# Kernel optimization log

Measured on AMD Instinct MI355X. Metric: run time of the kernel, lower is better.

The kernel has to match this reference:

```python
import jax, jax.numpy as jnp
import numpy as np

EPS = 1e-5  # pyg LayerNorm default eps


def _graph_ln(x):
    # pyg.nn.norm.LayerNorm(affine=False), default mode='graph', batch=None:
    # normalizes over ALL elements of the tensor (x - x.mean()) / x.std(unbiased=False)
    m = x.mean()
    v = jnp.mean((x - m) ** 2)
    return (x - m) * jax.lax.rsqrt(v + EPS)


def _cheb_conv(x, row, col, w, W, b):
    # ChebConv, normalization='sym', lambda_max=2 => scaled Laplacian
    # L_hat = L - I = -D^{-1/2} A D^{-1/2} (self-loops removed, weighted)
    # x: [B,N,C_in], row/col: [E], w: [E], W: [K,C_in,C_out], b: [C_out]
    N = x.shape[1]
    w = jnp.where(row == col, 0.0, w)  # remove_self_loops
    deg = jnp.zeros((N,), x.dtype).at[row].add(w)
    dinv = jnp.where(deg > 0, jax.lax.rsqrt(jnp.maximum(deg, 1e-12)), 0.0)
    norm = -(dinv[row] * w * dinv[col])  # [E]

    def prop(t):  # out[i] += norm_e * t[j] for edge (j=row -> i=col)
        msg = norm[None, :, None] * t[:, row, :]  # [B,E,C]
        return jnp.zeros_like(t).at[:, col, :].add(msg)

    Tx0 = x
    out = jnp.einsum('bnc,cd->bnd', Tx0, W[0])
    Tx1 = prop(x)
    out = out + jnp.einsum('bnc,cd->bnd', Tx1, W[1])
    for k in range(2, W.shape[0]):
        Tx2 = 2.0 * prop(Tx1) - Tx0
        out = out + jnp.einsum('bnc,cd->bnd', Tx2, W[k])
        Tx0, Tx1 = Tx1, Tx2
    return out + b


def setup_inputs() -> dict:
    key = jax.random.key(0)
    ks = jax.random.split(key, 8)
    B, N, C, E, L, K = 8, 2048, 256, 32768, 3, 3
    node_feature = jax.random.normal(ks[0], (B, N, C), dtype=jnp.float32)
    edge_index = jax.random.randint(ks[1], (L, 2, E), 0, N)
    edge_weight = jax.random.uniform(ks[2], (L, E), dtype=jnp.float32)
    s = 1.0 / np.sqrt(C)
    cheb_w = jax.random.normal(ks[3], (L, K, C, C), dtype=jnp.float32) * s
    cheb_b = jnp.zeros((L, C), dtype=jnp.float32)
    mlp_w = jax.random.normal(ks[4], (L, C, C), dtype=jnp.float32) * s
    mlp_b = jax.random.normal(ks[5], (L, C), dtype=jnp.float32) * 0.01
    return {"node_feature": node_feature, "edge_weight": edge_weight,
            "cheb_w": cheb_w, "cheb_b": cheb_b, "mlp_w": mlp_w,
            "mlp_b": mlp_b, "edge_index": edge_index}


def reference(node_feature, edge_weight, cheb_w, cheb_b, mlp_w, mlp_b, edge_index):
    h = node_feature  # [B,N,C]
    L = cheb_w.shape[0]
    for l in range(L):
        h_res = h
        hn = _graph_ln(h)
        hc = _cheb_conv(hn, edge_index[l, 0], edge_index[l, 1],
                        edge_weight[l], cheb_w[l], cheb_b[l])
        h = hc + h_res
        h_res = h
        hn = _graph_ln(h)
        hm = jax.nn.gelu(jnp.einsum('bnc,cd->bnd', hn, mlp_w[l]) + mlp_b[l],
                         approximate=False)  # dropout is identity at inference
        h = hm + h_res
    return h.mean(axis=1)  # [B,C]
```

## Files before the change

### kernel.cpp

```cpp
#include <hip/hip_runtime.h>

#define BATCH   8
#define NNODE   2048
#define CH      256
#define NEDGE   32768
#define NLAYER  3
#define MROWS   (NNODE*BATCH)
#define KCAT    (3*CH)
#define NTOT    (MROWS*CH)

typedef _Float16 half8 __attribute__((ext_vector_type(8)));
typedef _Float16 half4 __attribute__((ext_vector_type(4)));
typedef float    f32x4 __attribute__((ext_vector_type(4)));

#define OFF_H      ((size_t)0)
#define OFF_ACAT   ((size_t)16777216)
#define OFF_HF     ((size_t)41943040)
#define OFF_WT     ((size_t)50331648)
#define OFF_MT     ((size_t)51511296)
#define OFF_PARTA  ((size_t)51904512)
#define OFF_PARTB  ((size_t)51912704)
#define OFF_CS     ((size_t)51920896)
#define OFF_CSM    ((size_t)51930112)
#define OFF_DEG    ((size_t)51933184)
#define OFF_CNT    ((size_t)51957760)
#define OFF_ELIST  ((size_t)51982336)
#define OFF_NORM   ((size_t)53555200)
#define OFF_R1     ((size_t)53948416)
#define OFF_R2     ((size_t)53972992)
#define OFF_MP     ((size_t)53997568)

__device__ __forceinline__ void async_lds16(const void* g, void* l) {
  __builtin_amdgcn_global_load_lds((const __attribute__((address_space(1))) void*)g,
                                   (__attribute__((address_space(3))) void*)l, 16, 0, 0);
}

__global__ __launch_bounds__(256) void k_init(const float* __restrict__ x,
                                              float* __restrict__ h,
                                              _Float16* __restrict__ Acat,
                                              float2* __restrict__ part,
                                              float* __restrict__ deg,
                                              unsigned int* __restrict__ count,
                                              float* __restrict__ r1) {
  const int blk = blockIdx.x;
  if (blk < 1024) {
    int tid = blk*256 + threadIdx.x;
    float s = 0.f, s2 = 0.f;
    for (int i = tid; i < NTOT/4; i += 1024*256) {
      int c4 = i & 63, b = (i >> 6) & 7, n = i >> 9;
      float4 v = ((const float4*)x)[((b*NNODE + n) << 6) + c4];
      ((float4*)h)[i] = v;
      half4 o; o[0]=(_Float16)v.x; o[1]=(_Float16)v.y; o[2]=(_Float16)v.z; o[3]=(_Float16)v.w;
      *(half4*)&Acat[(size_t)(i >> 6)*KCAT + c4*4] = o;
      s  += v.x + v.y + v.z + v.w;
      s2 += v.x*v.x + v.y*v.y + v.z*v.z + v.w*v.w;
    }
    __shared__ float rs[512];
    rs[threadIdx.x] = s; rs[256+threadIdx.x] = s2; __syncthreads();
    for (int o = 128; o > 0; o >>= 1) {
      if (threadIdx.x < o) { rs[threadIdx.x] += rs[threadIdx.x+o]; rs[256+threadIdx.x] += rs[256+threadIdx.x+o]; }
      __syncthreads();
    }
    if (threadIdx.x == 0) part[blk] = make_float2(rs[0], rs[256]);
  } else {
    int i = (blk - 1024)*256 + threadIdx.x;
    if (i < NLAYER*NNODE) { deg[i] = 0.f; count[i] = 0u; r1[i] = 0.f; }
  }
}

__global__ __launch_bounds__(256) void k_weights(const float* __restrict__ cheb_w,
                                                 const float* __restrict__ mlp_w,
                                                 _Float16* __restrict__ Wt,
                                                 _Float16* __restrict__ Mt) {
  __shared__ _Float16 lt[64][72];
  const int t = threadIdx.x;
  const int rr = t >> 4, c4 = t & 15;
  const int tile = blockIdx.x;
  if (tile < 144) {
    const int l = tile / 48, rem = tile % 48;
    const int kk = rem / 16, q = rem % 16, ci = q >> 2, ni = q & 3;
    const float4* W  = (const float4*)cheb_w + ((size_t)((l*3 + kk)*CH + ci*64))*64 + ni*16;
    const float4* W2 = (const float4*)cheb_w + ((size_t)((l*3 + 2 )*CH + ci*64))*64 + ni*16;
    #pragma unroll
    for (int p = 0; p < 4; ++p) {
      const int r = p*16 + rr;
      float4 v = W[(size_t)r*64 + c4];
      if (kk == 0) {
        float4 v2 = W2[(size_t)r*64 + c4];
        v.x -= v2.x; v.y -= v2.y; v.z -= v2.z; v.w -= v2.w;
      } else if (kk == 2) {
        v.x *= 2.f; v.y *= 2.f; v.z *= 2.f; v.w *= 2.f;
      }
      lt[c4*4+0][r] = (_Float16)v.x; lt[c4*4+1][r] = (_Float16)v.y;
      lt[c4*4+2][r] = (_Float16)v.z; lt[c4*4+3][r] = (_Float16)v.w;
    }
    __syncthreads();
    const int nr = t >> 2, ch2 = t & 3;
    #pragma unroll
    for (int pp = 0; pp < 2; ++pp) {
      const int ch = ch2 + pp*4;
      half8 v = *(const half8*)&lt[nr][ch*8];
      *(half8*)&Wt[((size_t)(l*CH + ni*64 + nr))*KCAT + kk*256 + ci*64 + ch*8] = v;
    }
  } else {
    const int m = tile - 144;
    const int l = m / 16, q = m % 16, ci = q >> 2, ni = q & 3;
    const float4* W = (const float4*)mlp_w + ((size_t)(l*CH + ci*64))*64 + ni*16;
    #pragma unroll
    for (int p = 0; p < 4; ++p) {
      const int r = p*16 + rr;
      float4 v = W[(size_t)r*64 + c4];
      lt[c4*4+0][r] = (_Float16)v.x; lt[c4*4+1][r] = (_Float16)v.y;
      lt[c4*4+2][r] = (_Float16)v.z; lt[c4*4+3][r] = (_Float16)v.w;
    }
    __syncthreads();
    const int nr = t >> 2, ch2 = t & 3;
    #pragma unroll
    for (int pp = 0; pp < 2; ++pp) {
      const int ch = ch2 + pp*4;
      half8 v = *(const half8*)&lt[nr][ch*8];
      *(half8*)&Mt[((size_t)(l*CH + ni*64 + nr))*CH + ci*64 + ch*8] = v;
    }
  }
}

__global__ __launch_bounds__(256) void k_edge_scatter(const int* __restrict__ ei,
                                                      const float* __restrict__ ew,
                                                      float* deg, unsigned int* count,
                                                      unsigned int* elist) {
  int i = blockIdx.x*256 + threadIdx.x;
  if (i >= NLAYER*NEDGE) return;
  int l = i / NEDGE, e = i % NEDGE;
  const int* rows = ei + l*2*NEDGE;
  const int* cols = rows + NEDGE;
  int r = rows[e], c = cols[e];
  float w = (r == c) ? 0.f : ew[l*NEDGE + e];
  atomicAdd(&deg[l*NNODE + r], w);
  unsigned int slot = atomicAdd(&count[l*NNODE + c], 1u);
  if (slot < 64u) elist[(l*NNODE + c)*64 + slot] = (unsigned int)e;
}

__global__ __launch_bounds__(256) void k_edge_norm(const int* __restrict__ ei,
                                                   const float* __restrict__ ew,
                                                   const float* __restrict__ deg,
                                                   float* __restrict__ norm,
                                                   float* __restrict__ r1) {
  int i = blockIdx.x*256 + threadIdx.x;
  if (i >= NLAYER*NEDGE) return;
  int l = i / NEDGE, e = i % NEDGE;
  const int* rows = ei + l*2*NEDGE;
  const int* cols = rows + NEDGE;
  int r = rows[e], c = cols[e];
  float w = (r == c) ? 0.f : ew[l*NEDGE + e];
  float dr = deg[l*NNODE + r], dc = deg[l*NNODE + c];
  float ir = dr > 0.f ? rsqrtf(fmaxf(dr, 1e-12f)) : 0.f;
  float ic = dc > 0.f ? rsqrtf(fmaxf(dc, 1e-12f)) : 0.f;
  float nm = -(ir * w * ic);
  norm[i] = nm;
  atomicAdd(&r1[l*NNODE + c], nm);
}

__global__ __launch_bounds__(256) void k_aux(const int* __restrict__ ei,
                                             const float* __restrict__ norm,
                                             const unsigned int* __restrict__ count,
                                             const unsigned int* __restrict__ elist,
                                             const float* __restrict__ r1,
                                             float* __restrict__ r2,
                                             const _Float16* __restrict__ Wt,
                                             const _Float16* __restrict__ Mt,
                                             float* __restrict__ cs,
                                             float* __restrict__ csM) {
  const int blk = blockIdx.x;
  if (blk < 24) {
    int i = blk*256 + threadIdx.x;
    int l = i / NNODE;
    const int* rows = ei + l*2*NEDGE;
    unsigned int c = count[i]; if (c > 64u) c = 64u;
    const unsigned int* el = elist + (size_t)i*64;
    float s = 0.f;
    for (unsigned int j = 0; j < c; ++j) {
      unsigned int e = el[j];
      s += norm[l*NEDGE + e] * r1[l*NNODE + rows[e]];
    }
    r2[i] = s;
  } else if (blk < 33) {
    int idx = blk - 24;
    int l = idx / 3, kk = idx % 3, n = threadIdx.x;
    const half8* row = (const half8*)&Wt[((size_t)(l*CH + n))*KCAT + kk*256];
    float s = 0.f;
    #pragma unroll 4
    for (int j = 0; j < 32; ++j) {
      half8 v = row[j];
      s += (float)v[0]+(float)v[1]+(float)v[2]+(float)v[3]
         + (float)v[4]+(float)v[5]+(float)v[6]+(float)v[7];
    }
    cs[(l*3 + kk)*CH + n] = s;
  } else {
    int l = blk - 33, n = threadIdx.x;
    const half8* row = (const half8*)&Mt[((size_t)(l*CH + n))*CH];
    float s = 0.f;
    #pragma unroll 4
    for (int j = 0; j < 32; ++j) {
      half8 v = row[j];
      s += (float)v[0]+(float)v[1]+(float)v[2]+(float)v[3]
         + (float)v[4]+(float)v[5]+(float)v[6]+(float)v[7];
    }
    csM[l*CH + n] = s;
  }
}

template<int SRC_OFF, int DST_OFF>
__global__ __launch_bounds__(64) void k_prop(_Float16* __restrict__ Acat,
                                             const int* __restrict__ rows,
                                             const float* __restrict__ norm,
                                             const unsigned int* __restrict__ count,
                                             const unsigned int* __restrict__ elist) {
  const int blk = blockIdx.x;
  const int b = blk & 7, dst = blk >> 3;
  const int lane = threadIdx.x;
  unsigned int cnt = count[dst]; if (cnt > 64u) cnt = 64u;
  int   srcv = 0;
  float nmv  = 0.f;
  if (lane < (int)cnt) {
    unsigned int e = elist[dst*64 + lane];
    srcv = rows[e];
    nmv  = norm[e];
  }
  float a0 = 0.f, a1 = 0.f, a2 = 0.f, a3 = 0.f;
  const _Float16* base = Acat + SRC_OFF + lane*4;
  #define PROP_STEP(i)                                                              \
    {                                                                               \
      int   src = __builtin_amdgcn_readlane(srcv, (i));                             \
      int   nbi = __builtin_amdgcn_readlane(__builtin_bit_cast(int, nmv), (i));     \
      float nm  = __builtin_bit_cast(float, nbi);                                   \
      half4 v = *(const half4*)&base[(size_t)(src*8 + b)*KCAT];                     \
      a0 += nm*(float)v[0]; a1 += nm*(float)v[1];                                   \
      a2 += nm*(float)v[2]; a3 += nm*(float)v[3];                                   \
    }
  unsigned int i = 0;
  for (; i + 4 <= cnt; i += 4) { PROP_STEP(i) PROP_STEP(i+1) PROP_STEP(i+2) PROP_STEP(i+3) }
  for (; i < cnt; ++i) { PROP_STEP(i) }
  #undef PROP_STEP
  half4 o; o[0] = (_Float16)a0; o[1] = (_Float16)a1; o[2] = (_Float16)a2; o[3] = (_Float16)a3;
  *(half4*)&Acat[(size_t)(dst*8 + b)*KCAT + DST_OFF + lane*4] = o;
}

template<int KSTEPS, int DO_GELU>
__global__ __launch_bounds__(256) void k_gemm(const _Float16* __restrict__ A, int lda,
                                              const _Float16* __restrict__ Bt, int ldb,
                                              const float* __restrict__ bias,
                                              const float* __restrict__ cs,
                                              const float* __restrict__ r1,
                                              const float* __restrict__ r2,
                                              const float2* __restrict__ part_in,
                                              float2* __restrict__ part_out,
                                              float* __restrict__ H,
                                              _Float16* __restrict__ Of, int ofs) {
  __shared__ _Float16 Als[64*64];
  __shared__ _Float16 Bls[64*64];
  __shared__ float red[512];
  __shared__ float mv[2];
  const int bm = blockIdx.x, bn = blockIdx.y;
  const int t = threadIdx.x;
  const int w = t >> 6, lane = t & 63;
  const int quad = lane >> 4, l16 = lane & 15;
  const int wm = w & 1, wn = w >> 1;

  {
    float s = 0.f, s2 = 0.f;
    for (int i = t; i < 1024; i += 256) { float2 p = part_in[i]; s += p.x; s2 += p.y; }
    red[t] = s; red[256+t] = s2; __syncthreads();
    for (int o = 128; o > 0; o >>= 1) {
      if (t < o) { red[t] += red[t+o]; red[256+t] += red[256+t+o]; }
      __syncthreads();
    }
    if (t == 0) {
      float mean = red[0] * (1.f/(float)NTOT);
      float var  = red[256] * (1.f/(float)NTOT) - mean*mean;
      mv[0] = mean; mv[1] = rsqrtf(var + 1e-5f);
    }
    __syncthreads();
  }
  const float mean = mv[0], istd = mv[1];

  f32x4 acc00 = {0.f,0.f,0.f,0.f};
  f32x4 acc01 = acc00, acc10 = acc00, acc11 = acc00;

  const int c0 = w*64 + lane, c1 = 256 + w*64 + lane;
  const int r0 = c0 >> 3, s0 = (c0 & 7) ^ (r0 & 7);
  const int r1i = c1 >> 3, s1 = (c1 & 7) ^ (r1i & 7);
  const _Float16* ga0 = A  + (size_t)(bm*64 + r0)*lda + s0*8;
  const _Float16* ga1 = A  + (size_t)(bm*64 + r1i)*lda + s1*8;
  const _Float16* gb0 = Bt + (size_t)(bn*64 + r0)*ldb + s0*8;
  const _Float16* gb1 = Bt + (size_t)(bn*64 + r1i)*ldb + s1*8;
  _Float16* lA0 = &Als[w*512];
  _Float16* lA1 = &Als[2048 + w*512];
  _Float16* lB0 = &Bls[w*512];
  _Float16* lB1 = &Bls[2048 + w*512];

  const int ra0 = wm*32 + l16, ra1 = ra0 + 16;
  const int rb0 = wn*32 + l16, rb1 = rb0 + 16;

  for (int ks = 0; ks < KSTEPS; ++ks) {
    async_lds16(ga0, lA0); async_lds16(ga1, lA1);
    async_lds16(gb0, lB0); async_lds16(gb1, lB1);
    ga0 += 64; ga1 += 64; gb0 += 64; gb1 += 64;
    __syncthreads();
    #pragma unroll
    for (int kh = 0; kh < 2; ++kh) {
      const int q = kh*4 + quad;
      half8 a0 = *(const half8*)&Als[ra0*64 + (q ^ (ra0 & 7))*8];
      half8 a1 = *(const half8*)&Als[ra1*64 + (q ^ (ra1 & 7))*8];
      half8 b0 = *(const half8*)&Bls[rb0*64 + (q ^ (rb0 & 7))*8];
      half8 b1 = *(const half8*)&Bls[rb1*64 + (q ^ (rb1 & 7))*8];
      acc00 = __builtin_amdgcn_mfma_f32_16x16x32_f16(a0, b0, acc00, 0, 0, 0);
      acc01 = __builtin_amdgcn_mfma_f32_16x16x32_f16(a0, b1, acc01, 0, 0, 0);
      acc10 = __builtin_amdgcn_mfma_f32_16x16x32_f16(a1, b0, acc10, 0, 0, 0);
      acc11 = __builtin_amdgcn_mfma_f32_16x16x32_f16(a1, b1, acc11, 0, 0, 0);
    }
    __syncthreads();
  }

  float s = 0.f, s2 = 0.f;
  const int gm0 = bm*64 + wm*32, gn0 = bn*64 + wn*32;
  const float mi = -mean * istd;
  #pragma unroll
  for (int i = 0; i < 2; ++i) {
    #pragma unroll
    for (int j = 0; j < 2; ++j) {
      f32x4 a = (i == 0) ? (j == 0 ? acc00 : acc01) : (j == 0 ? acc10 : acc11);
      const int col = gn0 + j*16 + l16;
      const float bv = bias[col];
      const float c0v = cs[col];
      float c1v = 0.f, c2v = 0.f;
      if (!DO_GELU) { c1v = cs[256 + col]; c2v = cs[512 + col]; }
      #pragma unroll
      for (int r = 0; r < 4; ++r) {
        const int row = gm0 + i*16 + quad*4 + r;
        float v;
        if (DO_GELU) {
          v = istd*a[r] + mi*c0v + bv;
          v = 0.5f*v*(1.f + erff(v*0.70710678118654752f));
        } else {
          const int node = row >> 3;
          v = istd*a[r] + mi*(c0v + r1[node]*c1v + r2[node]*c2v) + bv;
        }
        float hv = H[(size_t)row*CH + col] + v;
        H[(size_t)row*CH + col] = hv;
        Of[(size_t)row*ofs + col] = (_Float16)hv;
        s += hv; s2 += hv*hv;
      }
    }
  }
  red[t] = s; red[256+t] = s2; __syncthreads();
  for (int o = 128; o > 0; o >>= 1) {
    if (t < o) { red[t] += red[t+o]; red[256+t] += red[256+t+o]; }
    __syncthreads();
  }
  if (t == 0) part_out[blockIdx.y*gridDim.x + blockIdx.x] = make_float2(red[0], red[256]);
}

__global__ __launch_bounds__(256) void k_mean_part(const float* __restrict__ h,
                                                   float* __restrict__ mp) {
  int blk = blockIdx.x;
  int b = blk & 7, chunk = blk >> 3;
  int c = threadIdx.x;
  float s = 0.f;
  for (int k = 0; k < 32; ++k) {
    int n = chunk*32 + k;
    s += h[((size_t)(n*8 + b) << 8) + c];
  }
  mp[((b*64 + chunk) << 8) + c] = s;
}

__global__ __launch_bounds__(256) void k_mean_final(const float* __restrict__ mp,
                                                    float* __restrict__ out) {
  int b = blockIdx.x, c = threadIdx.x;
  float s = 0.f;
  for (int ch = 0; ch < 64; ++ch) s += mp[((b*64 + ch) << 8) + c];
  out[(b << 8) + c] = s * (1.f/(float)NNODE);
}

extern "C" void kernel_launch(void* const* d_in, const int* in_sizes, int n_in,
                              void* d_out, int out_size, void* d_ws, size_t ws_size,
                              hipStream_t stream) {
  const float* x      = (const float*)d_in[0];
  const float* ew     = (const float*)d_in[1];
  const float* cheb_w = (const float*)d_in[2];
  const float* cheb_b = (const float*)d_in[3];
  const float* mlp_w  = (const float*)d_in[4];
  const float* mlp_b  = (const float*)d_in[5];
  const int*   ei     = (const int*)d_in[6];
  float* out = (float*)d_out;

  char* ws = (char*)d_ws;
  float*        h     = (float*)(ws + OFF_H);
  _Float16*     Acat  = (_Float16*)(ws + OFF_ACAT);
  _Float16*     Hf    = (_Float16*)(ws + OFF_HF);
  _Float16*     Wt    = (_Float16*)(ws + OFF_WT);
  _Float16*     Mt    = (_Float16*)(ws + OFF_MT);
  float2*       partA = (float2*)(ws + OFF_PARTA);
  float2*       partB = (float2*)(ws + OFF_PARTB);
  float*        cs    = (float*)(ws + OFF_CS);
  float*        csM   = (float*)(ws + OFF_CSM);
  float*        deg   = (float*)(ws + OFF_DEG);
  unsigned int* cnt   = (unsigned int*)(ws + OFF_CNT);
  unsigned int* elist = (unsigned int*)(ws + OFF_ELIST);
  float*        norm  = (float*)(ws + OFF_NORM);
  float*        r1    = (float*)(ws + OFF_R1);
  float*        r2    = (float*)(ws + OFF_R2);
  float*        mp    = (float*)(ws + OFF_MP);

  k_init<<<1048, 256, 0, stream>>>(x, h, Acat, partA, deg, cnt, r1);
  k_weights<<<192, 256, 0, stream>>>(cheb_w, mlp_w, Wt, Mt);
  k_edge_scatter<<<(NLAYER*NEDGE)/256, 256, 0, stream>>>(ei, ew, deg, cnt, elist);
  k_edge_norm<<<(NLAYER*NEDGE)/256, 256, 0, stream>>>(ei, ew, deg, norm, r1);
  k_aux<<<36, 256, 0, stream>>>(ei, norm, cnt, elist, r1, r2, Wt, Mt, cs, csM);

  for (int l = 0; l < NLAYER; ++l) {
    const int* rows_l = ei + l*2*NEDGE;
    const unsigned int* cnt_l = cnt + l*NNODE;
    const unsigned int* el_l  = elist + (size_t)l*NNODE*64;
    const float* norm_l = norm + l*NEDGE;

    k_prop<0, 256><<<MROWS, 64, 0, stream>>>(Acat, rows_l, norm_l, cnt_l, el_l);
    k_prop<256, 512><<<MROWS, 64, 0, stream>>>(Acat, rows_l, norm_l, cnt_l, el_l);
    k_gemm<12, 0><<<dim3(256, 4), 256, 0, stream>>>(
        Acat, KCAT, Wt + (size_t)l*CH*KCAT, KCAT, cheb_b + l*CH,
        cs + l*3*CH, r1 + l*NNODE, r2 + l*NNODE, partA, partB, h, Hf, CH);
    k_gemm<4, 1><<<dim3(256, 4), 256, 0, stream>>>(
        Hf, CH, Mt + (size_t)l*CH*CH, CH, mlp_b + l*CH,
        csM + l*CH, r1, r2, partB, partA, h, Acat, KCAT);
  }

  k_mean_part<<<512, 256, 0, stream>>>(h, mp);
  k_mean_final<<<8, 256, 0, stream>>>(mp, out);
}
```

Before: 317.3 us.

## Drop fp32 residual buffer, read residual from fp16, batch-group prop, merge weight prep

Removes the fp32 hidden-state buffer h. Residuals are now read from the fp16 copies already held in Acat and Hf, and the mean is taken from Acat, which cuts global read/write traffic in the GEMM epilogues. k_prop now has each wavefront handle four batches of one destination node, with 256-thread blocks, so the edge-list and readlane setup is shared. The weight-transpose kernel is folded into k_init to save a launch. The residual stream is now kept only in fp16, so rounding error builds up across layers.

```diff
diff --git a/kernel.cpp b/kernel.cpp
--- a/kernel.cpp
+++ b/kernel.cpp
@@ -13,22 +13,21 @@
 typedef _Float16 half4 __attribute__((ext_vector_type(4)));
 typedef float    f32x4 __attribute__((ext_vector_type(4)));
 
-#define OFF_H      ((size_t)0)
-#define OFF_ACAT   ((size_t)16777216)
-#define OFF_HF     ((size_t)41943040)
-#define OFF_WT     ((size_t)50331648)
-#define OFF_MT     ((size_t)51511296)
-#define OFF_PARTA  ((size_t)51904512)
-#define OFF_PARTB  ((size_t)51912704)
-#define OFF_CS     ((size_t)51920896)
-#define OFF_CSM    ((size_t)51930112)
-#define OFF_DEG    ((size_t)51933184)
-#define OFF_CNT    ((size_t)51957760)
-#define OFF_ELIST  ((size_t)51982336)
-#define OFF_NORM   ((size_t)53555200)
-#define OFF_R1     ((size_t)53948416)
-#define OFF_R2     ((size_t)53972992)
-#define OFF_MP     ((size_t)53997568)
+#define OFF_ACAT   ((size_t)0)
+#define OFF_HF     ((size_t)25165824)
+#define OFF_WT     ((size_t)33554432)
+#define OFF_MT     ((size_t)34734080)
+#define OFF_PARTA  ((size_t)35127296)
+#define OFF_PARTB  ((size_t)35135488)
+#define OFF_CS     ((size_t)35143680)
+#define OFF_CSM    ((size_t)35152896)
+#define OFF_DEG    ((size_t)35155968)
+#define OFF_CNT    ((size_t)35180544)
+#define OFF_ELIST  ((size_t)35205120)
+#define OFF_NORM   ((size_t)36777984)
+#define OFF_R1     ((size_t)37171200)
+#define OFF_R2     ((size_t)37195776)
+#define OFF_MP     ((size_t)37220352)
 
 __device__ __forceinline__ void async_lds16(const void* g, void* l) {
   __builtin_amdgcn_global_load_lds((const __attribute__((address_space(1))) void*)g,
@@ -36,90 +35,86 @@
 }
 
 __global__ __launch_bounds__(256) void k_init(const float* __restrict__ x,
-                                              float* __restrict__ h,
                                               _Float16* __restrict__ Acat,
                                               float2* __restrict__ part,
+                                              const float* __restrict__ cheb_w,
+                                              const float* __restrict__ mlp_w,
+                                              _Float16* __restrict__ Wt,
+                                              _Float16* __restrict__ Mt,
                                               float* __restrict__ deg,
                                               unsigned int* __restrict__ count,
                                               float* __restrict__ r1) {
-  const int blk = blockIdx.x;
+  __shared__ float rs[512];
+  __shared__ _Float16 lt[64][72];
+  const int blk = blockIdx.x, t = threadIdx.x;
   if (blk < 1024) {
-    int tid = blk*256 + threadIdx.x;
+    int tid = blk*256 + t;
     float s = 0.f, s2 = 0.f;
     for (int i = tid; i < NTOT/4; i += 1024*256) {
       int c4 = i & 63, b = (i >> 6) & 7, n = i >> 9;
       float4 v = ((const float4*)x)[((b*NNODE + n) << 6) + c4];
-      ((float4*)h)[i] = v;
       half4 o; o[0]=(_Float16)v.x; o[1]=(_Float16)v.y; o[2]=(_Float16)v.z; o[3]=(_Float16)v.w;
       *(half4*)&Acat[(size_t)(i >> 6)*KCAT + c4*4] = o;
       s  += v.x + v.y + v.z + v.w;
       s2 += v.x*v.x + v.y*v.y + v.z*v.z + v.w*v.w;
     }
-    __shared__ float rs[512];
-    rs[threadIdx.x] = s; rs[256+threadIdx.x] = s2; __syncthreads();
+    rs[t] = s; rs[256+t] = s2; __syncthreads();
     for (int o = 128; o > 0; o >>= 1) {
-      if (threadIdx.x < o) { rs[threadIdx.x] += rs[threadIdx.x+o]; rs[256+threadIdx.x] += rs[256+threadIdx.x+o]; }
+      if (t < o) { rs[t] += rs[t+o]; rs[256+t] += rs[256+t+o]; }
       __syncthreads();
     }
-    if (threadIdx.x == 0) part[blk] = make_float2(rs[0], rs[256]);
+    if (t == 0) part[blk] = make_float2(rs[0], rs[256]);
+  } else if (blk < 1048) {
+    int i = (blk - 1024)*256 + t;
+    if (i < NLAYER*NNODE) { deg[i] = 0.f; count[i] = 0u; r1[i] = 0.f; }
   } else {
-    int i = (blk - 1024)*256 + threadIdx.x;
-    if (i < NLAYER*NNODE) { deg[i] = 0.f; count[i] = 0u; r1[i] = 0.f; }
-  }
-}
-
-__global__ __launch_bounds__(256) void k_weights(const float* __restrict__ cheb_w,
-                                                 const float* __restrict__ mlp_w,
-                                                 _Float16* __restrict__ Wt,
-                                                 _Float16* __restrict__ Mt) {
-  __shared__ _Float16 lt[64][72];
-  const int t = threadIdx.x;
-  const int rr = t >> 4, c4 = t & 15;
-  const int tile = blockIdx.x;
-  if (tile < 144) {
-    const int l = tile / 48, rem = tile % 48;
-    const int kk = rem / 16, q = rem % 16, ci = q >> 2, ni = q & 3;
-    const float4* W  = (const float4*)cheb_w + ((size_t)((l*3 + kk)*CH + ci*64))*64 + ni*16;
-    const float4* W2 = (const float4*)cheb_w + ((size_t)((l*3 + 2 )*CH + ci*64))*64 + ni*16;
-    #pragma unroll
-    for (int p = 0; p < 4; ++p) {
-      const int r = p*16 + rr;
-      float4 v = W[(size_t)r*64 + c4];
-      if (kk == 0) {
-        float4 v2 = W2[(size_t)r*64 + c4];
-        v.x -= v2.x; v.y -= v2.y; v.z -= v2.z; v.w -= v2.w;
-      } else if (kk == 2) {
-        v.x *= 2.f; v.y *= 2.f; v.z *= 2.f; v.w *= 2.f;
+    const int tile = blk - 1048;
+    const int rr = t >> 4, c4 = t & 15;
+    if (tile < 144) {
+      const int l = tile / 48, rem = tile % 48;
+      const int kk = rem / 16, q = rem % 16, ci = q >> 2, ni = q & 3;
+      const float4* W  = (const float4*)cheb_w + ((size_t)((l*3 + kk)*CH + ci*64))*64 + ni*16;
+      const float4* W2 = (const float4*)cheb_w + ((size_t)((l*3 + 2 )*CH + ci*64))*64 + ni*16;
+      #pragma unroll
+      for (int p = 0; p < 4; ++p) {
+        const int r = p*16 + rr;
+        float4 v = W[(size_t)r*64 + c4];
+        if (kk == 0) {
+          float4 v2 = W2[(size_t)r*64 + c4];
+          v.x -= v2.x; v.y -= v2.y; v.z -= v2.z; v.w -= v2.w;
+        } else if (kk == 2) {
+          v.x *= 2.f; v.y *= 2.f; v.z *= 2.f; v.w *= 2.f;
+        }
+        lt[c4*4+0][r] = (_Float16)v.x; lt[c4*4+1][r] = (_Float16)v.y;
+        lt[c4*4+2][r] = (_Float16)v.z; lt[c4*4+3][r] = (_Float16)v.w;
       }
-      lt[c4*4+0][r] = (_Float16)v.x; lt[c4*4+1][r] = (_Float16)v.y;
-      lt[c4*4+2][r] = (_Float16)v.z; lt[c4*4+3][r] = (_Float16)v.w;
-    }
-    __syncthreads();
-    const int nr = t >> 2, ch2 = t & 3;
-    #pragma unroll
-    for (int pp = 0; pp < 2; ++pp) {
-      const int ch = ch2 + pp*4;
-      half8 v = *(const half8*)&lt[nr][ch*8];
-      *(half8*)&Wt[((size_t)(l*CH + ni*64 + nr))*KCAT + kk*256 + ci*64 + ch*8] = v;
-    }
-  } else {
-    const int m = tile - 144;
-    const int l = m / 16, q = m % 16, ci = q >> 2, ni = q & 3;
-    const float4* W = (const float4*)mlp_w + ((size_t)(l*CH + ci*64))*64 + ni*16;
-    #pragma unroll
-    for (int p = 0; p < 4; ++p) {
-      const int r = p*16 + rr;
-      float4 v = W[(size_t)r*64 + c4];
-      lt[c4*4+0][r] = (_Float16)v.x; lt[c4*4+1][r] = (_Float16)v.y;
-      lt[c4*4+2][r] = (_Float16)v.z; lt[c4*4+3][r] = (_Float16)v.w;
-    }
-    __syncthreads();
-    const int nr = t >> 2, ch2 = t & 3;
-    #pragma unroll
-    for (int pp = 0; pp < 2; ++pp) {
-      const int ch = ch2 + pp*4;
-      half8 v = *(const half8*)&lt[nr][ch*8];
-      *(half8*)&Mt[((size_t)(l*CH + ni*64 + nr))*CH + ci*64 + ch*8] = v;
+      __syncthreads();
+      const int nr = t >> 2, ch2 = t & 3;
+      #pragma unroll
+      for (int pp = 0; pp < 2; ++pp) {
+        const int ch = ch2 + pp*4;
+        half8 v = *(const half8*)&lt[nr][ch*8];
+        *(half8*)&Wt[((size_t)(l*CH + ni*64 + nr))*KCAT + kk*256 + ci*64 + ch*8] = v;
+      }
+    } else {
+      const int m = tile - 144;
+      const int l = m / 16, q = m % 16, ci = q >> 2, ni = q & 3;
+      const float4* W = (const float4*)mlp_w + ((size_t)(l*CH + ci*64))*64 + ni*16;
+      #pragma unroll
+      for (int p = 0; p < 4; ++p) {
+        const int r = p*16 + rr;
+        float4 v = W[(size_t)r*64 + c4];
+        lt[c4*4+0][r] = (_Float16)v.x; lt[c4*4+1][r] = (_Float16)v.y;
+        lt[c4*4+2][r] = (_Float16)v.z; lt[c4*4+3][r] = (_Float16)v.w;
+      }
+      __syncthreads();
+      const int nr = t >> 2, ch2 = t & 3;
+      #pragma unroll
+      for (int pp = 0; pp < 2; ++pp) {
+        const int ch = ch2 + pp*4;
+        half8 v = *(const half8*)&lt[nr][ch*8];
+        *(half8*)&Mt[((size_t)(l*CH + ni*64 + nr))*CH + ci*64 + ch*8] = v;
+      }
     }
   }
 }
@@ -134,10 +129,10 @@
   const int* rows = ei + l*2*NEDGE;
   const int* cols = rows + NEDGE;
   int r = rows[e], c = cols[e];
-  float w = (r == c) ? 0.f : ew[l*NEDGE + e];
+  float w = (r == c) ? 0.f : ew[i];
   atomicAdd(&deg[l*NNODE + r], w);
   unsigned int slot = atomicAdd(&count[l*NNODE + c], 1u);
-  if (slot < 64u) elist[(l*NNODE + c)*64 + slot] = (unsigned int)e;
+  if (slot < 64u) elist[(size_t)(l*NNODE + c)*64 + slot] = (unsigned int)e;
 }
 
 __global__ __launch_bounds__(256) void k_edge_norm(const int* __restrict__ ei,
@@ -151,7 +146,7 @@
   const int* rows = ei + l*2*NEDGE;
   const int* cols = rows + NEDGE;
   int r = rows[e], c = cols[e];
-  float w = (r == c) ? 0.f : ew[l*NEDGE + e];
+  float w = (r == c) ? 0.f : ew[i];
   float dr = deg[l*NNODE + r], dc = deg[l*NNODE + c];
   float ir = dr > 0.f ? rsqrtf(fmaxf(dr, 1e-12f)) : 0.f;
   float ic = dc > 0.f ? rsqrtf(fmaxf(dc, 1e-12f)) : 0.f;
@@ -210,39 +205,40 @@
 }
 
 template<int SRC_OFF, int DST_OFF>
-__global__ __launch_bounds__(64) void k_prop(_Float16* __restrict__ Acat,
-                                             const int* __restrict__ rows,
-                                             const float* __restrict__ norm,
-                                             const unsigned int* __restrict__ count,
-                                             const unsigned int* __restrict__ elist) {
-  const int blk = blockIdx.x;
-  const int b = blk & 7, dst = blk >> 3;
-  const int lane = threadIdx.x;
-  unsigned int cnt = count[dst]; if (cnt > 64u) cnt = 64u;
-  int   srcv = 0;
-  float nmv  = 0.f;
-  if (lane < (int)cnt) {
-    unsigned int e = elist[dst*64 + lane];
-    srcv = rows[e];
-    nmv  = norm[e];
-  }
-  float a0 = 0.f, a1 = 0.f, a2 = 0.f, a3 = 0.f;
+__global__ __launch_bounds__(256) void k_prop(_Float16* __restrict__ Acat,
+                                              const int* __restrict__ rows,
+                                              const float* __restrict__ nrm,
+                                              const unsigned int* __restrict__ count,
+                                              const unsigned int* __restrict__ el) {
+  const int g = blockIdx.x*4 + (threadIdx.x >> 6);
+  const int lane = threadIdx.x & 63;
+  const int dst = g >> 1, bb = (g & 1) << 2;
+  unsigned int c = count[dst]; if (c > 64u) c = 64u;
+  int srcv = 0; float nmv = 0.f;
+  if (lane < (int)c) {
+    unsigned int e = el[(size_t)dst*64 + lane];
+    srcv = rows[e]; nmv = nrm[e];
+  }
+  float acc[4][4] = {{0.f,0.f,0.f,0.f},{0.f,0.f,0.f,0.f},{0.f,0.f,0.f,0.f},{0.f,0.f,0.f,0.f}};
   const _Float16* base = Acat + SRC_OFF + lane*4;
-  #define PROP_STEP(i)                                                              \
-    {                                                                               \
-      int   src = __builtin_amdgcn_readlane(srcv, (i));                             \
-      int   nbi = __builtin_amdgcn_readlane(__builtin_bit_cast(int, nmv), (i));     \
-      float nm  = __builtin_bit_cast(float, nbi);                                   \
-      half4 v = *(const half4*)&base[(size_t)(src*8 + b)*KCAT];                     \
-      a0 += nm*(float)v[0]; a1 += nm*(float)v[1];                                   \
-      a2 += nm*(float)v[2]; a3 += nm*(float)v[3];                                   \
-    }
-  unsigned int i = 0;
-  for (; i + 4 <= cnt; i += 4) { PROP_STEP(i) PROP_STEP(i+1) PROP_STEP(i+2) PROP_STEP(i+3) }
-  for (; i < cnt; ++i) { PROP_STEP(i) }
-  #undef PROP_STEP
-  half4 o; o[0] = (_Float16)a0; o[1] = (_Float16)a1; o[2] = (_Float16)a2; o[3] = (_Float16)a3;
-  *(half4*)&Acat[(size_t)(dst*8 + b)*KCAT + DST_OFF + lane*4] = o;
+  for (unsigned int i = 0; i < c; ++i) {
+    int   src = __builtin_amdgcn_readlane(srcv, i);
+    int   nbi = __builtin_amdgcn_readlane(__builtin_bit_cast(int, nmv), i);
+    float nm  = __builtin_bit_cast(float, nbi);
+    const _Float16* p = base + (size_t)(src*8 + bb)*KCAT;
+    #pragma unroll
+    for (int j = 0; j < 4; ++j) {
+      half4 v = *(const half4*)(p + (size_t)j*KCAT);
+      acc[j][0] += nm*(float)v[0]; acc[j][1] += nm*(float)v[1];
+      acc[j][2] += nm*(float)v[2]; acc[j][3] += nm*(float)v[3];
+    }
+  }
+  #pragma unroll
+  for (int j = 0; j < 4; ++j) {
+    half4 o; o[0]=(_Float16)acc[j][0]; o[1]=(_Float16)acc[j][1];
+    o[2]=(_Float16)acc[j][2]; o[3]=(_Float16)acc[j][3];
+    *(half4*)&Acat[(size_t)(dst*8 + bb + j)*KCAT + DST_OFF + lane*4] = o;
+  }
 }
 
 template<int KSTEPS, int DO_GELU>
@@ -254,8 +250,8 @@
                                               const float* __restrict__ r2,
                                               const float2* __restrict__ part_in,
                                               float2* __restrict__ part_out,
-                                              float* __restrict__ H,
-                                              _Float16* __restrict__ Of, int ofs) {
+                                              const _Float16* __restrict__ R, int ldr,
+                                              _Float16* __restrict__ O, int ldo) {
   __shared__ _Float16 Als[64*64];
   __shared__ _Float16 Bls[64*64];
   __shared__ float red[512];
@@ -345,9 +341,8 @@
           const int node = row >> 3;
           v = istd*a[r] + mi*(c0v + r1[node]*c1v + r2[node]*c2v) + bv;
         }
-        float hv = H[(size_t)row*CH + col] + v;
-        H[(size_t)row*CH + col] = hv;
-        Of[(size_t)row*ofs + col] = (_Float16)hv;
+        float hv = (float)R[(size_t)row*ldr + col] + v;
+        O[(size_t)row*ldo + col] = (_Float16)hv;
         s += hv; s2 += hv*hv;
       }
     }
@@ -360,7 +355,7 @@
   if (t == 0) part_out[blockIdx.y*gridDim.x + blockIdx.x] = make_float2(red[0], red[256]);
 }
 
-__global__ __launch_bounds__(256) void k_mean_part(const float* __restrict__ h,
+__global__ __launch_bounds__(256) void k_mean_part(const _Float16* __restrict__ Acat,
                                                    float* __restrict__ mp) {
   int blk = blockIdx.x;
   int b = blk & 7, chunk = blk >> 3;
@@ -368,7 +363,7 @@
   float s = 0.f;
   for (int k = 0; k < 32; ++k) {
     int n = chunk*32 + k;
-    s += h[((size_t)(n*8 + b) << 8) + c];
+    s += (float)Acat[(size_t)(n*8 + b)*KCAT + c];
   }
   mp[((b*64 + chunk) << 8) + c] = s;
 }
@@ -394,7 +389,6 @@
   float* out = (float*)d_out;
 
   char* ws = (char*)d_ws;
-  float*        h     = (float*)(ws + OFF_H);
   _Float16*     Acat  = (_Float16*)(ws + OFF_ACAT);
   _Float16*     Hf    = (_Float16*)(ws + OFF_HF);
   _Float16*     Wt    = (_Float16*)(ws + OFF_WT);
@@ -411,8 +405,7 @@
   float*        r2    = (float*)(ws + OFF_R2);
   float*        mp    = (float*)(ws + OFF_MP);
 
-  k_init<<<1048, 256, 0, stream>>>(x, h, Acat, partA, deg, cnt, r1);
-  k_weights<<<192, 256, 0, stream>>>(cheb_w, mlp_w, Wt, Mt);
+  k_init<<<1240, 256, 0, stream>>>(x, Acat, partA, cheb_w, mlp_w, Wt, Mt, deg, cnt, r1);
   k_edge_scatter<<<(NLAYER*NEDGE)/256, 256, 0, stream>>>(ei, ew, deg, cnt, elist);
   k_edge_norm<<<(NLAYER*NEDGE)/256, 256, 0, stream>>>(ei, ew, deg, norm, r1);
   k_aux<<<36, 256, 0, stream>>>(ei, norm, cnt, elist, r1, r2, Wt, Mt, cs, csM);
@@ -423,16 +416,18 @@
     const unsigned int* el_l  = elist + (size_t)l*NNODE*64;
     const float* norm_l = norm + l*NEDGE;
 
-    k_prop<0, 256><<<MROWS, 64, 0, stream>>>(Acat, rows_l, norm_l, cnt_l, el_l);
-    k_prop<256, 512><<<MROWS, 64, 0, stream>>>(Acat, rows_l, norm_l, cnt_l, el_l);
+    k_prop<0, 256><<<1024, 256, 0, stream>>>(Acat, rows_l, norm_l, cnt_l, el_l);
+    k_prop<256, 512><<<1024, 256, 0, stream>>>(Acat, rows_l, norm_l, cnt_l, el_l);
     k_gemm<12, 0><<<dim3(256, 4), 256, 0, stream>>>(
         Acat, KCAT, Wt + (size_t)l*CH*KCAT, KCAT, cheb_b + l*CH,
-        cs + l*3*CH, r1 + l*NNODE, r2 + l*NNODE, partA, partB, h, Hf, CH);
+        cs + l*3*CH, r1 + l*NNODE, r2 + l*NNODE, partA, partB,
+        Acat, KCAT, Hf, CH);
     k_gemm<4, 1><<<dim3(256, 4), 256, 0, stream>>>(
         Hf, CH, Mt + (size_t)l*CH*CH, CH, mlp_b + l*CH,
-        csM + l*CH, r1, r2, partB, partA, h, Acat, KCAT);
-  }
-
-  k_mean_part<<<512, 256, 0, stream>>>(h, mp);
+        csM + l*CH, r1, r2, partB, partA,
+        Hf, CH, Acat, KCAT);
+  }
+
+  k_mean_part<<<512, 256, 0, stream>>>(Acat, mp);
   k_mean_final<<<8, 256, 0, stream>>>(mp, out);
 }
```

Result: no change. 315.0 us (-0.7%).
